# Performance work log

Hardware: AMD Instinct MI355X
Metric: run time of the kernel (lower is better)

## Reference

```python
import jax, jax.numpy as jnp
import numpy as np


def _sobel_kernels(dtype):
    # Faithful to the torch code: each kernel has shape (1,3,3) in (kd,kh,kw),
    # i.e. a 2D Sobel applied slice-wise, but conv3d uses padding=1 on ALL dims
    # so the output depth is D+2.
    sx = np.array([[[-1, 0, 1], [-2, 0, 2], [-1, 0, 1]]], dtype=np.float32)  # (1,3,3)
    sy = np.transpose(sx, (0, 2, 1))                                          # transpose(1,2)
    sz = np.array([[[-1, -2, -1], [0, 0, 0], [1, 2, 1]]], dtype=np.float32)
    k = np.stack([sx, sy, sz])[:, None]  # (3 out, 1 in, 1, 3, 3)
    return jnp.asarray(k, dtype)


def setup_inputs() -> dict:
    key = jax.random.key(0)
    k1, k2 = jax.random.split(key)
    B, C, D, H, W = 2, 4, 96, 160, 160
    pred = jax.random.normal(k1, (B, C, D, H, W), dtype=jnp.float32)
    target = jax.random.randint(k2, (B, D, H, W), 0, C)
    return {"pred": pred, "target": target}


def reference(pred, target):
    B, C, D, H, W = pred.shape
    p = jax.nn.softmax(pred, axis=1)                                   # (B,C,D,H,W)
    t = jax.nn.one_hot(target, C, dtype=pred.dtype)                    # (B,D,H,W,C)
    t = jnp.transpose(t, (0, 4, 1, 2, 3))                              # (B,C,D,H,W)
    k = _sobel_kernels(pred.dtype)

    def sobel(x):
        # fold class into batch; 3 output channels = x/y/z gradients
        x = x.reshape(B * C, 1, D, H, W)
        return jax.lax.conv_general_dilated(
            x, k, window_strides=(1, 1, 1), padding=[(1, 1)] * 3,
            dimension_numbers=("NCDHW", "OIDHW", "NCDHW"))           # (B*C,3,D+2,H+2,W+2)

    diff = sobel(p) - sobel(t)
    # Each torch mse_loss averages over a (B,1,D+2,H+2,W+2) tensor; the 3*C
    # means are summed, then divided by num_classes.
    per_tensor = B * (D + 2) * (H + 2) * (W + 2)
    loss = jnp.sum(diff * diff) / per_tensor / C
    return loss
```

## Files before the change

### kernel.cpp

```cpp
#include <hip/hip_runtime.h>

#define NB 2
#define NC 4
#define ND 96
#define NH 160
#define NW 160

constexpr int TW = 64, TH = 32;
constexpr int SW = TW + 2, SH = TH + 2;
constexpr int NSTRIP = 3;
constexpr int NCH = NH / TH;
constexpr int RPT = TH / 4;
constexpr float SCALE = 1.0f / (2.0f * 98.0f * 162.0f * 162.0f * 4.0f);

__global__ __launch_bounds__(256) void boundary_loss_kernel(
    const float* __restrict__ pred,
    const int*   __restrict__ target,
    float* __restrict__ out)
{
    __shared__ float4 q4[SH * SW];
    __shared__ float wsum[4];

    const int tid   = threadIdx.x;
    const int slice = blockIdx.y;
    const int b     = slice / ND;
    const int d     = slice - b * ND;
    const int tile  = blockIdx.x;
    const int strip = tile % NSTRIP;
    const int chunk = tile / NSTRIP;
    const int x0    = strip * TW;
    const int y0    = chunk * TH;

    const size_t cs    = (size_t)ND * NH * NW;
    const size_t pbase = ((size_t)b * NC * ND + d) * (size_t)(NH * NW);
    const size_t tbase = ((size_t)b * ND + d) * (size_t)(NH * NW);

    for (int idx = tid; idx < SH * SW; idx += 256) {
        const int r  = idx / SW;
        const int c  = idx - r * SW;
        const int gh = y0 + r - 1;
        const int gw = x0 + c - 1;
        float4 v = make_float4(0.f, 0.f, 0.f, 0.f);
        if (gh >= 0 && gh < NH && gw >= 0 && gw < NW) {
            const size_t off = pbase + (size_t)gh * NW + gw;
            const float p0 = pred[off];
            const float p1 = pred[off + cs];
            const float p2 = pred[off + 2 * cs];
            const float p3 = pred[off + 3 * cs];
            const int   tg = target[tbase + (size_t)gh * NW + gw];
            const float m  = fmaxf(fmaxf(p0, p1), fmaxf(p2, p3));
            const float e0 = __expf(p0 - m);
            const float e1 = __expf(p1 - m);
            const float e2 = __expf(p2 - m);
            const float e3 = __expf(p3 - m);
            const float inv = 1.0f / (e0 + e1 + e2 + e3);
            v.x = e0 * inv - (tg == 0 ? 1.f : 0.f);
            v.y = e1 * inv - (tg == 1 ? 1.f : 0.f);
            v.z = e2 * inv - (tg == 2 ? 1.f : 0.f);
            v.w = e3 * inv - (tg == 3 ? 1.f : 0.f);
        }
        q4[idx] = v;
    }
    __syncthreads();

    const int lane = tid & 63;
    const int grp  = tid >> 6;
    const int cc   = lane + 1;
    const int r0   = grp * RPT;

    float smm[NC], sm[NC], dmm[NC], dm[NC];
    #pragma unroll
    for (int c = 0; c < NC; ++c) { smm[c] = sm[c] = dmm[c] = dm[c] = 0.f; }

    float acc = 0.f;
    #pragma unroll
    for (int t = 0; t < RPT + 2; ++t) {
        const int base = (r0 + t) * SW + cc;
        const float4 ql = q4[base - 1];
        const float4 qm = q4[base];
        const float4 qr = q4[base + 1];
        const float* lf = (const float*)&ql;
        const float* mf = (const float*)&qm;
        const float* rf = (const float*)&qr;
        #pragma unroll
        for (int c = 0; c < NC; ++c) {
            const float sn = lf[c] + 2.f * mf[c] + rf[c];
            const float dn = rf[c] - lf[c];
            if (t >= 2) {
                const float gx = dmm[c] + 2.f * dm[c] + dn;
                const float gy = sn - smm[c];
                acc += gx * gx + 2.f * gy * gy;
            }
            smm[c] = sm[c]; sm[c] = sn;
            dmm[c] = dm[c]; dm[c] = dn;
        }
    }

    #pragma unroll
    for (int off = 32; off > 0; off >>= 1)
        acc += __shfl_down(acc, off, 64);
    if (lane == 0) wsum[grp] = acc;
    __syncthreads();
    if (tid == 0) {
        const float s = wsum[0] + wsum[1] + wsum[2] + wsum[3];
        atomicAdd(out, s * SCALE);
    }
}

extern "C" void kernel_launch(void* const* d_in, const int* in_sizes, int n_in,
                              void* d_out, int out_size, void* d_ws, size_t ws_size,
                              hipStream_t stream) {
    const float* pred   = (const float*)d_in[0];
    const int*   target = (const int*)d_in[1];
    float*       out    = (float*)d_out;

    hipMemsetAsync(out, 0, sizeof(float), stream);

    dim3 grid(NSTRIP * NCH, NB * ND);
    boundary_loss_kernel<<<grid, 256, 0, stream>>>(pred, target, out);
}
```

Baseline: 154.0 us.

## Use full-width row bands with float4 loads and swizzled LDS staging

Each block now covers a full-width band of 8 rows (plus halo), so the horizontal halo and the padded tile columns go away. Global reads become float4 per class plus int4 targets, with each thread staging up to two 4-pixel slots. Shared memory uses an XOR-like cell swizzle to avoid bank conflicts on the 4-wide writes. The trade-off is a larger vertical halo ratio (10 rows loaded per 8 output rows, so more redundant softmax), and only 160 of 256 threads do the stencil phase.

```diff
diff --git a/kernel.cpp b/kernel.cpp
--- a/kernel.cpp
+++ b/kernel.cpp
@@ -6,100 +6,138 @@
 #define NH 160
 #define NW 160
 
-constexpr int TW = 64, TH = 32;
-constexpr int SW = TW + 2, SH = TH + 2;
-constexpr int NSTRIP = 3;
-constexpr int NCH = NH / TH;
-constexpr int RPT = TH / 4;
+constexpr int TH    = 8;
+constexpr int SR    = TH + 2;
+constexpr int NBAND = NH / TH;
+constexpr int PITCH = NW;
+constexpr int NCELL = SR * PITCH;
+constexpr int NSLOT = NCELL / 4;
 constexpr float SCALE = 1.0f / (2.0f * 98.0f * 162.0f * 162.0f * 4.0f);
 
-__global__ __launch_bounds__(256) void boundary_loss_kernel(
+__device__ __forceinline__ int cell(int i) {
+    return (i & ~3) | ((i + (i >> 2)) & 3);
+}
+
+__device__ __forceinline__ void stage_slot(float4* __restrict__ q4s,
+                                           const float4* p, const int4& tg,
+                                           bool valid, int flat0) {
+    #pragma unroll
+    for (int k = 0; k < 4; ++k) {
+        float4 v = make_float4(0.f, 0.f, 0.f, 0.f);
+        if (valid) {
+            const float p0 = ((const float*)&p[0])[k];
+            const float p1 = ((const float*)&p[1])[k];
+            const float p2 = ((const float*)&p[2])[k];
+            const float p3 = ((const float*)&p[3])[k];
+            const int   t  = ((const int*)&tg)[k];
+            const float m  = fmaxf(fmaxf(p0, p1), fmaxf(p2, p3));
+            const float e0 = __expf(p0 - m);
+            const float e1 = __expf(p1 - m);
+            const float e2 = __expf(p2 - m);
+            const float e3 = __expf(p3 - m);
+            const float inv = 1.0f / (e0 + e1 + e2 + e3);
+            v.x = e0 * inv - (t == 0 ? 1.f : 0.f);
+            v.y = e1 * inv - (t == 1 ? 1.f : 0.f);
+            v.z = e2 * inv - (t == 2 ? 1.f : 0.f);
+            v.w = e3 * inv - (t == 3 ? 1.f : 0.f);
+        }
+        q4s[cell(flat0 + k)] = v;
+    }
+}
+
+__global__ __launch_bounds__(256, 6) void boundary_loss_kernel(
     const float* __restrict__ pred,
     const int*   __restrict__ target,
     float* __restrict__ out)
 {
-    __shared__ float4 q4[SH * SW];
+    __shared__ float4 q4s[NCELL];
     __shared__ float wsum[4];
 
     const int tid   = threadIdx.x;
     const int slice = blockIdx.y;
     const int b     = slice / ND;
     const int d     = slice - b * ND;
-    const int tile  = blockIdx.x;
-    const int strip = tile % NSTRIP;
-    const int chunk = tile / NSTRIP;
-    const int x0    = strip * TW;
-    const int y0    = chunk * TH;
+    const int y0    = blockIdx.x * TH;
 
-    const size_t cs    = (size_t)ND * NH * NW;
+    const size_t cs4   = (size_t)ND * NH * NW / 4;
     const size_t pbase = ((size_t)b * NC * ND + d) * (size_t)(NH * NW);
     const size_t tbase = ((size_t)b * ND + d) * (size_t)(NH * NW);
 
-    for (int idx = tid; idx < SH * SW; idx += 256) {
-        const int r  = idx / SW;
-        const int c  = idx - r * SW;
-        const int gh = y0 + r - 1;
-        const int gw = x0 + c - 1;
-        float4 v = make_float4(0.f, 0.f, 0.f, 0.f);
-        if (gh >= 0 && gh < NH && gw >= 0 && gw < NW) {
-            const size_t off = pbase + (size_t)gh * NW + gw;
-            const float p0 = pred[off];
-            const float p1 = pred[off + cs];
-            const float p2 = pred[off + 2 * cs];
-            const float p3 = pred[off + 3 * cs];
-            const int   tg = target[tbase + (size_t)gh * NW + gw];
-            const float m  = fmaxf(fmaxf(p0, p1), fmaxf(p2, p3));
-            const float e0 = __expf(p0 - m);
-            const float e1 = __expf(p1 - m);
-            const float e2 = __expf(p2 - m);
-            const float e3 = __expf(p3 - m);
-            const float inv = 1.0f / (e0 + e1 + e2 + e3);
-            v.x = e0 * inv - (tg == 0 ? 1.f : 0.f);
-            v.y = e1 * inv - (tg == 1 ? 1.f : 0.f);
-            v.z = e2 * inv - (tg == 2 ? 1.f : 0.f);
-            v.w = e3 * inv - (tg == 3 ? 1.f : 0.f);
-        }
-        q4[idx] = v;
+    const int  rA   = tid / 40;
+    const int  cA   = tid - rA * 40;
+    const int  gyA  = y0 - 1 + rA;
+    const bool vA   = (gyA >= 0) && (gyA < NH);
+    const int  gyAc = min(max(gyA, 0), NH - 1);
+
+    const int  sB   = tid + 256;
+    const bool hasB = (sB < NSLOT);
+    const int  rB   = sB / 40;
+    const int  cB   = sB - rB * 40;
+    const int  gyB  = y0 - 1 + rB;
+    const bool vB   = hasB && (gyB >= 0) && (gyB < NH);
+    const int  gyBc = min(max(gyB, 0), NH - 1);
+
+    float4 pA[4], pB[4];
+    int4   tA = make_int4(0, 0, 0, 0), tB = make_int4(0, 0, 0, 0);
+    {
+        const float4* pp = (const float4*)(pred + pbase + (size_t)gyAc * NW) + cA;
+        pA[0] = pp[0];
+        pA[1] = pp[cs4];
+        pA[2] = pp[2 * cs4];
+        pA[3] = pp[3 * cs4];
+        tA = ((const int4*)(target + tbase + (size_t)gyAc * NW))[cA];
     }
+    if (hasB) {
+        const float4* pp = (const float4*)(pred + pbase + (size_t)gyBc * NW) + cB;
+        pB[0] = pp[0];
+        pB[1] = pp[cs4];
+        pB[2] = pp[2 * cs4];
+        pB[3] = pp[3 * cs4];
+        tB = ((const int4*)(target + tbase + (size_t)gyBc * NW))[cB];
+    } else {
+        pB[0] = pB[1] = pB[2] = pB[3] = make_float4(0.f, 0.f, 0.f, 0.f);
+    }
+
+    stage_slot(q4s, pA, tA, vA, rA * PITCH + 4 * cA);
+    if (hasB) stage_slot(q4s, pB, tB, vB, rB * PITCH + 4 * cB);
     __syncthreads();
 
-    const int lane = tid & 63;
-    const int grp  = tid >> 6;
-    const int cc   = lane + 1;
-    const int r0   = grp * RPT;
+    float acc = 0.f;
+    if (tid < NW) {
+        float smm[NC], sm[NC], dmm[NC], dm[NC];
+        #pragma unroll
+        for (int c = 0; c < NC; ++c) { smm[c] = sm[c] = dmm[c] = dm[c] = 0.f; }
 
-    float smm[NC], sm[NC], dmm[NC], dm[NC];
-    #pragma unroll
-    for (int c = 0; c < NC; ++c) { smm[c] = sm[c] = dmm[c] = dm[c] = 0.f; }
-
-    float acc = 0.f;
-    #pragma unroll
-    for (int t = 0; t < RPT + 2; ++t) {
-        const int base = (r0 + t) * SW + cc;
-        const float4 ql = q4[base - 1];
-        const float4 qm = q4[base];
-        const float4 qr = q4[base + 1];
-        const float* lf = (const float*)&ql;
-        const float* mf = (const float*)&qm;
-        const float* rf = (const float*)&qr;
         #pragma unroll
-        for (int c = 0; c < NC; ++c) {
-            const float sn = lf[c] + 2.f * mf[c] + rf[c];
-            const float dn = rf[c] - lf[c];
-            if (t >= 2) {
-                const float gx = dmm[c] + 2.f * dm[c] + dn;
-                const float gy = sn - smm[c];
-                acc += gx * gx + 2.f * gy * gy;
+        for (int t = 0; t < SR; ++t) {
+            const int base = t * PITCH + tid;
+            const float4 qm = q4s[cell(base)];
+            float4 ql = make_float4(0.f, 0.f, 0.f, 0.f);
+            float4 qr = make_float4(0.f, 0.f, 0.f, 0.f);
+            if (tid > 0)      ql = q4s[cell(base - 1)];
+            if (tid < NW - 1) qr = q4s[cell(base + 1)];
+            const float* lf = (const float*)&ql;
+            const float* mf = (const float*)&qm;
+            const float* rf = (const float*)&qr;
+            #pragma unroll
+            for (int c = 0; c < NC; ++c) {
+                const float sn = lf[c] + 2.f * mf[c] + rf[c];
+                const float dn = rf[c] - lf[c];
+                if (t >= 2) {
+                    const float gx = dmm[c] + 2.f * dm[c] + dn;
+                    const float gy = sn - smm[c];
+                    acc += gx * gx + 2.f * gy * gy;
+                }
+                smm[c] = sm[c]; sm[c] = sn;
+                dmm[c] = dm[c]; dm[c] = dn;
             }
-            smm[c] = sm[c]; sm[c] = sn;
-            dmm[c] = dm[c]; dm[c] = dn;
         }
     }
 
     #pragma unroll
     for (int off = 32; off > 0; off >>= 1)
         acc += __shfl_down(acc, off, 64);
-    if (lane == 0) wsum[grp] = acc;
+    if ((tid & 63) == 0) wsum[tid >> 6] = acc;
     __syncthreads();
     if (tid == 0) {
         const float s = wsum[0] + wsum[1] + wsum[2] + wsum[3];
@@ -116,6 +154,6 @@
 
     hipMemsetAsync(out, 0, sizeof(float), stream);
 
-    dim3 grid(NSTRIP * NCH, NB * ND);
+    dim3 grid(NBAND, NB * ND);
     boundary_loss_kernel<<<grid, 256, 0, stream>>>(pred, target, out);
 }
```

Result: slower. 184.3 us (+19.7%).
